# Optimization experiments

Measured on AMD Instinct MI355X. Metric: run time of the kernel, lower is better.

Reference implementation:

```python
import jax, jax.numpy as jnp
import numpy as np

DIM = 384
HEADS = 6
HD = DIM // HEADS
PATCH = 2
FR = 0.5
HEXP = int(HEADS * 4.0)       # attn_proj expanded heads
PR = DIM // 4                  # SQA proj1 out dim
HID = DIM * 4                  # MLP hidden
EPS = 1e-5
SCALE = 1.0 / np.sqrt(HD).astype(np.float32)


def _ln(x, w, b):
    m = jnp.mean(x, axis=-1, keepdims=True)
    v = jnp.var(x, axis=-1, keepdims=True)
    return (x - m) / jnp.sqrt(v + EPS) * w + b


def _lin(x, w, b):
    return x @ w.T + b


def setup_inputs() -> dict:
    key = jax.random.key(0)
    ks = jax.random.split(key, 16)
    def p(i, shape, s=0.02):
        return jax.random.normal(ks[i], shape, jnp.float32) * s
    return {
        "x": jax.random.normal(ks[0], (3136, DIM), jnp.float32),
        "qa": jax.random.normal(ks[1], (1, DIM), jnp.float32),
        "conv_w": p(2, (DIM, 1, 3, 3), 0.1),
        "conv_b": jnp.zeros((DIM,), jnp.float32),
        "norm1_w": jnp.ones((DIM,), jnp.float32),
        "norm1_b": jnp.zeros((DIM,), jnp.float32),
        "norm2_w": jnp.ones((DIM,), jnp.float32),
        "norm2_b": jnp.zeros((DIM,), jnp.float32),
        "qkv_w": p(3, (3 * DIM, DIM)),
        "qkv_b": jnp.zeros((3 * DIM,), jnp.float32),
        "mproj_w": p(4, (DIM, DIM)),
        "mproj_b": jnp.zeros((DIM,), jnp.float32),
        "ap1_w": p(5, (HEXP, HEADS), 0.1),
        "ap1_b": jnp.zeros((HEXP,), jnp.float32),
        "ap2_w": p(6, (HEADS, HEXP), 0.1),
        "ap2_b": jnp.zeros((HEADS,), jnp.float32),
        "kv_w": p(7, (2 * DIM, DIM)),
        "kv_b": jnp.zeros((2 * DIM,), jnp.float32),
        "sp1_w": p(8, (PR, DIM)),
        "sp1_b": jnp.zeros((PR,), jnp.float32),
        "sp2_w": p(9, (DIM, PR)),
        "sp2_b": jnp.zeros((DIM,), jnp.float32),
        "pn_w": jnp.ones((PR,), jnp.float32),
        "pn_b": jnp.zeros((PR,), jnp.float32),
        "fc1_w": p(10, (HID, DIM)),
        "fc1_b": jnp.zeros((HID,), jnp.float32),
        "fc2_w": p(11, (DIM, HID)),
        "fc2_b": jnp.zeros((DIM,), jnp.float32),
    }


def _mmsa(x, qkv_w, qkv_b, mproj_w, mproj_b, ap1_w, ap1_b, ap2_w, ap2_b):
    # x: [S, DIM]
    s = x.shape[0]
    qkv = _lin(x, qkv_w, qkv_b).reshape(s, 3, HEADS, HD).transpose(1, 2, 0, 3)  # [3,h,s,d]
    q, k, v = qkv[0], qkv[1], qkv[2]
    attn = jnp.einsum('hqd,hkd->hqk', q, k) * SCALE           # [h,q,k]
    a = attn.transpose(1, 2, 0)                                # [q,k,h]
    a = a @ ap1_w.T + ap1_b                                    # [q,k,hexp]
    a = jax.nn.softmax(a, axis=1)                              # softmax over k (axis=1)
    a = a @ ap2_w.T + ap2_b                                    # [q,k,h]
    attn = a.transpose(2, 0, 1)                                # [h,q,k]
    out = jnp.einsum('hqk,hkd->hqd', attn, v)
    out = out.transpose(1, 0, 2).reshape(s, DIM)
    return _lin(out, mproj_w, mproj_b)


def _sqa(x, q, kv_w, kv_b, sp1_w, sp1_b, sp2_w, sp2_b, pn_w, pn_b):
    # x: [S, DIM], q: [1, DIM]
    s = x.shape[0]
    qh = q.reshape(1, HEADS, HD).transpose(1, 0, 2)            # [h,1,d]
    kv = _lin(x, kv_w, kv_b).reshape(s, 2, HEADS, HD).transpose(1, 2, 0, 3)
    k, v = kv[0], kv[1]
    attn = jax.nn.softmax(jnp.einsum('hqd,hkd->hqk', qh, k) * SCALE, axis=-1)
    x1 = jnp.einsum('hqk,hkd->hqd', attn, v).transpose(1, 0, 2).reshape(1, DIM)
    x1 = jax.nn.relu(_ln(_lin(x1, sp1_w, sp1_b), pn_w, pn_b))
    x1 = _lin(x1, sp2_w, sp2_b)
    return x + x1                                              # broadcast residual over S


def reference(x, qa, conv_w, conv_b, norm1_w, norm1_b, norm2_w, norm2_b,
              qkv_w, qkv_b, mproj_w, mproj_b, ap1_w, ap1_b, ap2_w, ap2_b,
              kv_w, kv_b, sp1_w, sp1_b, sp2_w, sp2_b, pn_w, pn_b,
              fc1_w, fc1_b, fc2_w, fc2_b):
    L = x.shape[0]
    Hs = int(np.sqrt(L)); Ws = Hs
    # PosCNN2D: depthwise 3x3 conv + residual
    xi = x.T.reshape(1, DIM, Hs, Ws)
    conv = jax.lax.conv_general_dilated(xi, conv_w, (1, 1), 'SAME', feature_group_count=DIM)
    xi = conv + conv_b[None, :, None, None] + xi
    c = xi[0]                                                  # [DIM,Hs,Ws]
    hp, wp = Hs // PATCH, Ws // PATCH
    # 'c (h h1) (w w1) -> (h w) (h1 w1) c'
    x1 = c.reshape(DIM, hp, PATCH, wp, PATCH).transpose(1, 3, 2, 4, 0).reshape(hp * wp, PATCH * PATCH, DIM)
    n = hp * wp
    nf = int(n * FR)
    means = x1.mean(axis=(1, 2))
    idx = jnp.argsort(-means)                                  # descending
    nf_idx, nb_idx = idx[:nf], idx[nf:]
    f = x1[nf_idx].reshape(nf * PATCH * PATCH, DIM)
    b = x1[nb_idx].reshape((n - nf) * PATCH * PATCH, DIM)
    qf = _mmsa(jnp.concatenate([qa, f], axis=0),
               qkv_w, qkv_b, mproj_w, mproj_b, ap1_w, ap1_b, ap2_w, ap2_b)
    qa2, f = qf[:1], qf[1:]
    b = _sqa(b, qa2, kv_w, kv_b, sp1_w, sp1_b, sp2_w, sp2_b, pn_w, pn_b)
    # scatter foreground/background back to patch order
    x1n = jnp.zeros_like(x1)
    x1n = x1n.at[nf_idx].set(f.reshape(nf, PATCH * PATCH, DIM))
    x1n = x1n.at[nb_idx].set(b.reshape(n - nf, PATCH * PATCH, DIM))
    # inverse rearrange '(h w) (h1 w1) c -> ((h h1)(w w1)) c'
    x1f = x1n.reshape(hp, wp, PATCH, PATCH, DIM).transpose(0, 2, 1, 3, 4).reshape(L, DIM)
    x = x + _ln(x1f, norm1_w, norm1_b)
    h = _ln(x, norm2_w, norm2_b)
    h = jax.nn.silu(_lin(h, fc1_w, fc1_b))
    x = x + _lin(h, fc2_w, fc2_b)
    return x, qa2
```

## Files before the change

### kernel.cpp

```cpp
#include <hip/hip_runtime.h>
#include <hip/hip_bf16.h>

#define DIM 384
#define HEADS 6
#define HD 64
#define LPIX 3136
#define HS 56
#define NPATCH 784
#define NF 392
#define SEQ 1569
#define BROWS 1568
#define HEXP 24
#define PR 96
#define HID 1536
#define SCALE 0.125f
#define EPSV 1e-5f
#define KPAD 1576
#define QSTR 9456

typedef short short8v __attribute__((ext_vector_type(8)));
typedef float f32x4 __attribute__((ext_vector_type(4)));
typedef unsigned short ushort;

__device__ __forceinline__ ushort f2b(float f) {
    __hip_bfloat16 h = __float2bfloat16(f);
    return reinterpret_cast<ushort&>(h);
}
__device__ __forceinline__ float b2f(ushort u) {
    unsigned int ui = ((unsigned int)u) << 16;
    return __uint_as_float(ui);
}

struct CvtSeg { const float* s; ushort* d; int n; };
__global__ __launch_bounds__(256) void cvt_kernel(CvtSeg a, CvtSeg b, CvtSeg c, CvtSeg d, CvtSeg e) {
    CvtSeg seg;
    switch (blockIdx.y) { case 0: seg = a; break; case 1: seg = b; break; case 2: seg = c; break;
                          case 3: seg = d; break; default: seg = e; break; }
    int idx = (blockIdx.x * 256 + threadIdx.x) * 8;
    if (idx >= seg.n) return;
    float4 f0 = *reinterpret_cast<const float4*>(seg.s + idx);
    float4 f1 = *reinterpret_cast<const float4*>(seg.s + idx + 4);
    ushort u[8] = { f2b(f0.x), f2b(f0.y), f2b(f0.z), f2b(f0.w),
                    f2b(f1.x), f2b(f1.y), f2b(f1.z), f2b(f1.w) };
    *reinterpret_cast<uint4*>(seg.d + idx) = *reinterpret_cast<uint4*>(u);
}

__global__ __launch_bounds__(384) void conv_kernel(const float* __restrict__ x,
                                                   const float* __restrict__ cw,
                                                   const float* __restrict__ cb,
                                                   float* __restrict__ x1) {
    int l = blockIdx.x, c = threadIdx.x;
    int hh = l / HS, ww = l % HS;
    float acc = x[(long)l * DIM + c] + cb[c];
    #pragma unroll
    for (int kh = 0; kh < 3; kh++) {
        int h2 = hh + kh - 1;
        if (h2 < 0 || h2 >= HS) continue;
        #pragma unroll
        for (int kw = 0; kw < 3; kw++) {
            int w2 = ww + kw - 1;
            if (w2 < 0 || w2 >= HS) continue;
            acc += x[((long)h2 * HS + w2) * DIM + c] * cw[c * 9 + kh * 3 + kw];
        }
    }
    int p = (hh >> 1) * 28 + (ww >> 1);
    int t = ((hh & 1) << 1) | (ww & 1);
    x1[(long)(p * 4 + t) * DIM + c] = acc;
}

__global__ __launch_bounds__(256) void means_kernel(const float* __restrict__ x1, float* __restrict__ means) {
    int p = blockIdx.x, tid = threadIdx.x;
    __shared__ float red[256];
    float s = 0.f;
    for (int i = tid; i < 1536; i += 256) s += x1[(long)p * 1536 + i];
    red[tid] = s; __syncthreads();
    for (int k = 128; k > 0; k >>= 1) { if (tid < k) red[tid] += red[tid + k]; __syncthreads(); }
    if (tid == 0) means[p] = red[0] / 1536.f;
}

__global__ __launch_bounds__(256) void partition_flags_kernel(const float* __restrict__ means, int* __restrict__ flags) {
    int p = blockIdx.x * 256 + threadIdx.x;
    if (p >= NPATCH) return;
    float m = means[p];
    int rank = 0;
    for (int q = 0; q < NPATCH; q++) {
        float mq = means[q];
        rank += (mq > m) || (mq == m && q < p);
    }
    flags[p] = (rank < NF) ? 1 : 0;
}

__global__ __launch_bounds__(256) void partition_compact_kernel(const int* __restrict__ flags, int* __restrict__ isfg,
                                                                int* __restrict__ pos, int* __restrict__ fgmap,
                                                                int* __restrict__ bgmap) {
    __shared__ int f_s[NPATCH];
    __shared__ int scan_s[256];
    int tid = threadIdx.x;
    for (int p = tid; p < NPATCH; p += 256) f_s[p] = flags[p];
    __syncthreads();
    int base = tid * 4, cnt = 0;
    #pragma unroll
    for (int i = 0; i < 4; i++) { int p = base + i; if (p < NPATCH) cnt += f_s[p]; }
    scan_s[tid] = cnt; __syncthreads();
    for (int off = 1; off < 256; off <<= 1) {
        int add = (tid >= off) ? scan_s[tid - off] : 0;
        __syncthreads();
        scan_s[tid] += add;
        __syncthreads();
    }
    int run = scan_s[tid] - cnt;
    for (int i = 0; i < 4; i++) {
        int p = base + i;
        if (p >= NPATCH) break;
        int f = f_s[p];
        if (f) { isfg[p] = 1; pos[p] = run; fgmap[run] = p; run++; }
        else   { isfg[p] = 0; pos[p] = p - run; bgmap[p - run] = p; }
    }
}

__global__ __launch_bounds__(384) void gather_kernel(const float* __restrict__ x1, const float* __restrict__ qa,
                                                     const int* __restrict__ fgmap, const int* __restrict__ bgmap,
                                                     ushort* __restrict__ Xmsa_bf, float* __restrict__ B,
                                                     ushort* __restrict__ B_bf) {
    int c = threadIdx.x;
    int bid = blockIdx.x;
    if (bid == 0) { Xmsa_bf[c] = f2b(qa[c]); return; }
    if (bid <= BROWS) {
        int r = bid - 1;
        int src = fgmap[r >> 2] * 4 + (r & 3);
        Xmsa_bf[(long)bid * DIM + c] = f2b(x1[(long)src * DIM + c]);
    } else {
        int r = bid - SEQ;
        int src = bgmap[r >> 2] * 4 + (r & 3);
        float v = x1[(long)src * DIM + c];
        B[(long)r * DIM + c] = v;
        B_bf[(long)r * DIM + c] = f2b(v);
    }
}

template<int BM, int BN, int OPB, int ACT, int OUTBF>
__global__ __launch_bounds__(256) void mgemm(
    const ushort* __restrict__ A, int lda, long long sA,
    const ushort* __restrict__ B, int ldb, long long sB,
    const float* __restrict__ bias, const float* __restrict__ resid, int ldr,
    void* __restrict__ Cv, int ldc, long long sC,
    int M, int N, int K, float alpha) {
    constexpr int BK = 32, LDT = BK + 8;
    constexpr int WR = (BM == 128 && BN == 128) ? 2 : ((BM == 128) ? 4 : 2);
    constexpr int WC = 4 / WR;
    constexpr int MFR = BM / WR / 16;
    constexpr int NFR = BN / WC / 16;
    __shared__ ushort As[BM * LDT];
    __shared__ ushort Bs[BN * LDT];
    int tid = threadIdx.x;
    int wid = tid >> 6, lane = tid & 63;
    int m0 = blockIdx.y * BM, n0 = blockIdx.x * BN;
    int bz = blockIdx.z;
    A += (long long)bz * sA;
    B += (long long)bz * sB;
    int wm = (wid / WC) * (BM / WR);
    int wn = (wid % WC) * (BN / WC);
    f32x4 acc[MFR][NFR];
    #pragma unroll
    for (int mi = 0; mi < MFR; mi++)
        #pragma unroll
        for (int ni = 0; ni < NFR; ni++) acc[mi][ni] = (f32x4){0.f, 0.f, 0.f, 0.f};

    for (int k0 = 0; k0 < K; k0 += BK) {
        {
            constexpr int CHA = BM * 4 / 256;
            #pragma unroll
            for (int t = 0; t < CHA; t++) {
                int chunk = tid + t * 256;
                int row = chunk >> 2, part = chunk & 3;
                int gm = m0 + row, gk = k0 + part * 8;
                ushort* dst = &As[row * LDT + part * 8];
                if (gm < M && gk + 8 <= K) {
                    *reinterpret_cast<uint4*>(dst) =
                        *reinterpret_cast<const uint4*>(&A[(long long)gm * lda + gk]);
                } else {
                    #pragma unroll
                    for (int i = 0; i < 8; i++) {
                        int k = gk + i;
                        dst[i] = (gm < M && k < K) ? A[(long long)gm * lda + k] : (ushort)0;
                    }
                }
            }
        }
        if (OPB == 1) {
            constexpr int CHB = BN * 4 / 256;
            #pragma unroll
            for (int t = 0; t < CHB; t++) {
                int chunk = tid + t * 256;
                int row = chunk >> 2, part = chunk & 3;
                int gn = n0 + row, gk = k0 + part * 8;
                ushort* dst = &Bs[row * LDT + part * 8];
                if (gn < N && gk + 8 <= K) {
                    *reinterpret_cast<uint4*>(dst) =
                        *reinterpret_cast<const uint4*>(&B[(long long)gn * ldb + gk]);
                } else {
                    #pragma unroll
                    for (int i = 0; i < 8; i++) {
                        int k = gk + i;
                        dst[i] = (gn < N && k < K) ? B[(long long)gn * ldb + k] : (ushort)0;
                    }
                }
            }
        } else {
            int kr = tid >> 3, nn = (tid & 7) * 8;
            int gk = k0 + kr;
            ushort vals[8];
            if (gk < K && n0 + nn + 8 <= N) {
                *reinterpret_cast<uint4*>(vals) =
                    *reinterpret_cast<const uint4*>(&B[(long long)gk * ldb + n0 + nn]);
            } else {
                #pragma unroll
                for (int i = 0; i < 8; i++) {
                    int gn = n0 + nn + i;
                    vals[i] = (gk < K && gn < N) ? B[(long long)gk * ldb + gn] : (ushort)0;
                }
            }
            #pragma unroll
            for (int i = 0; i < 8; i++) Bs[(nn + i) * LDT + kr] = vals[i];
        }
        __syncthreads();
        short8v a[MFR], b[NFR];
        #pragma unroll
        for (int mi = 0; mi < MFR; mi++)
            a[mi] = *reinterpret_cast<const short8v*>(&As[(wm + mi * 16 + (lane & 15)) * LDT + (lane >> 4) * 8]);
        #pragma unroll
        for (int ni = 0; ni < NFR; ni++)
            b[ni] = *reinterpret_cast<const short8v*>(&Bs[(wn + ni * 16 + (lane & 15)) * LDT + (lane >> 4) * 8]);
        #pragma unroll
        for (int mi = 0; mi < MFR; mi++)
            #pragma unroll
            for (int ni = 0; ni < NFR; ni++)
                acc[mi][ni] = __builtin_amdgcn_mfma_f32_16x16x32_bf16(a[mi], b[ni], acc[mi][ni], 0, 0, 0);
        __syncthreads();
    }
    ushort* C16 = (ushort*)Cv;
    float* C32 = (float*)Cv;
    #pragma unroll
    for (int mi = 0; mi < MFR; mi++) {
        #pragma unroll
        for (int j = 0; j < 4; j++) {
            int gm = m0 + wm + mi * 16 + (lane >> 4) * 4 + j;
            if (gm >= M) continue;
            #pragma unroll
            for (int ni = 0; ni < NFR; ni++) {
                int gn = n0 + wn + ni * 16 + (lane & 15);
                if (gn >= N) continue;
                float v = acc[mi][ni][j] * alpha;
                if (bias) v += bias[gn];
                if (ACT == 1) v = v / (1.f + __expf(-v));
                if (resid) v += resid[(long long)gm * ldr + gn];
                long long ci = bz * sC + (long long)gm * ldc + gn;
                if (OUTBF) C16[ci] = f2b(v); else C32[ci] = v;
            }
        }
    }
}

__global__ __launch_bounds__(512, 2) void modattn_kernel(
    ushort* __restrict__ S,
    const float* __restrict__ ap1_w, const float* __restrict__ ap1_b,
    const float* __restrict__ ap2_w, const float* __restrict__ ap2_b) {
    int q = blockIdx.x, tid = threadIdx.x;
    int wid = tid >> 6, lane = tid & 63;
    __shared__ float w1s[144], w2s[144], b1s[24], b2s[6];
    __shared__ float red[8][24];
    __shared__ float fin[24];
    if (tid < 144) { w1s[tid] = ap1_w[tid]; w2s[tid] = ap2_w[tid]; }
    if (tid < 24) b1s[tid] = ap1_b[tid];
    if (tid < 6)  b2s[tid] = ap2_b[tid];
    __syncthreads();
    ushort* Sq = S + (long long)q * QSTR;
    float sreg[4][6];
    #pragma unroll
    for (int j = 0; j < 4; j++) {
        int k = tid + j * 512;
        #pragma unroll
        for (int h = 0; h < 6; h++)
            sreg[j][h] = (k < SEQ) ? b2f(Sq[h * KPAD + k]) : 0.f;
    }
    float a1[4][24];
    float r24[24];
    #pragma unroll
    for (int e = 0; e < 24; e++) r24[e] = -3.4e38f;
    #pragma unroll
    for (int j = 0; j < 4; j++) {
        int k = tid + j * 512;
        bool v = k < SEQ;
        #pragma unroll
        for (int e = 0; e < 24; e++) {
            float a = b1s[e];
            #pragma unroll
            for (int h = 0; h < 6; h++) a = fmaf(sreg[j][h], w1s[e * 6 + h], a);
            a1[j][e] = a;
            if (v) r24[e] = fmaxf(r24[e], a);
        }
    }
    #pragma unroll
    for (int e = 0; e < 24; e++) {
        float v = r24[e];
        #pragma unroll
        for (int off = 32; off >= 1; off >>= 1) v = fmaxf(v, __shfl_xor(v, off));
        r24[e] = v;
    }
    if (lane == 0) {
        #pragma unroll
        for (int e = 0; e < 24; e++) red[wid][e] = r24[e];
    }
    __syncthreads();
    if (tid < 24) {
        float v = red[0][tid];
        #pragma unroll
        for (int w = 1; w < 8; w++) v = fmaxf(v, red[w][tid]);
        fin[tid] = v;
    }
    __syncthreads();
    #pragma unroll
    for (int e = 0; e < 24; e++) r24[e] = 0.f;
    #pragma unroll
    for (int j = 0; j < 4; j++) {
        int k = tid + j * 512;
        bool v = k < SEQ;
        #pragma unroll
        for (int e = 0; e < 24; e++) {
            float p = v ? __expf(a1[j][e] - fin[e]) : 0.f;
            a1[j][e] = p;
            r24[e] += p;
        }
    }
    #pragma unroll
    for (int e = 0; e < 24; e++) {
        float v = r24[e];
        #pragma unroll
        for (int off = 32; off >= 1; off >>= 1) v += __shfl_xor(v, off);
        r24[e] = v;
    }
    __syncthreads();
    if (lane == 0) {
        #pragma unroll
        for (int e = 0; e < 24; e++) red[wid][e] = r24[e];
    }
    __syncthreads();
    if (tid < 24) {
        float v = red[0][tid];
        #pragma unroll
        for (int w = 1; w < 8; w++) v += red[w][tid];
        fin[tid] = 1.f / v;
    }
    __syncthreads();
    #pragma unroll
    for (int j = 0; j < 4; j++) {
        int k = tid + j * 512;
        if (k >= SEQ) continue;
        float a2[6];
        #pragma unroll
        for (int h = 0; h < 6; h++) a2[h] = b2s[h];
        #pragma unroll
        for (int e = 0; e < 24; e++) {
            float p = a1[j][e] * fin[e];
            #pragma unroll
            for (int h = 0; h < 6; h++) a2[h] = fmaf(p, w2s[h * 24 + e], a2[h]);
        }
        #pragma unroll
        for (int h = 0; h < 6; h++) Sq[h * KPAD + k] = f2b(a2[h]);
    }
}

__global__ __launch_bounds__(256) void sqa_attn_kernel(const float* __restrict__ kv, const float* __restrict__ qa2,
                                                       float* __restrict__ x1h) {
    int h = blockIdx.x, tid = threadIdx.x;
    __shared__ float q_s[HD];
    __shared__ float l_s[BROWS];
    __shared__ float red[256];
    if (tid < HD) q_s[tid] = qa2[h * HD + tid];
    __syncthreads();
    float lmax = -1e30f;
    for (int s = tid; s < BROWS; s += 256) {
        const float* krow = kv + (long long)s * 768 + h * HD;
        float d = 0.f;
        for (int i = 0; i < HD; i++) d += krow[i] * q_s[i];
        d *= SCALE; l_s[s] = d; lmax = fmaxf(lmax, d);
    }
    red[tid] = lmax; __syncthreads();
    for (int s = 128; s > 0; s >>= 1) { if (tid < s) red[tid] = fmaxf(red[tid], red[tid + s]); __syncthreads(); }
    float gmax = red[0]; __syncthreads();
    float lsum = 0.f;
    for (int s = tid; s < BROWS; s += 256) { float p = __expf(l_s[s] - gmax); l_s[s] = p; lsum += p; }
    red[tid] = lsum; __syncthreads();
    for (int s = 128; s > 0; s >>= 1) { if (tid < s) red[tid] += red[tid + s]; __syncthreads(); }
    float inv = 1.f / red[0]; __syncthreads();
    int d = tid & 63, g = tid >> 6;
    float acc = 0.f;
    for (int s = g; s < BROWS; s += 4) acc += l_s[s] * kv[(long long)s * 768 + 384 + h * HD + d];
    red[tid] = acc; __syncthreads();
    if (tid < HD) x1h[h * HD + d] = (red[d] + red[64 + d] + red[128 + d] + red[192 + d]) * inv;
}

__global__ __launch_bounds__(384) void sqa_mlp_kernel(const float* __restrict__ x1h,
                                                      const float* __restrict__ sp1_w, const float* __restrict__ sp1_b,
                                                      const float* __restrict__ pn_w, const float* __restrict__ pn_b,
                                                      const float* __restrict__ sp2_w, const float* __restrict__ sp2_b,
                                                      float* __restrict__ z) {
    __shared__ float y_s[PR];
    __shared__ float x_s[DIM];
    __shared__ float mv[2];
    int tid = threadIdx.x;
    x_s[tid] = x1h[tid];
    __syncthreads();
    if (tid < PR) {
        float a = sp1_b[tid];
        for (int c = 0; c < DIM; c++) a += sp1_w[tid * DIM + c] * x_s[c];
        y_s[tid] = a;
    }
    __syncthreads();
    if (tid == 0) {
        float m = 0.f; for (int i = 0; i < PR; i++) m += y_s[i]; m /= (float)PR;
        float v = 0.f; for (int i = 0; i < PR; i++) { float d = y_s[i] - m; v += d * d; } v /= (float)PR;
        mv[0] = m; mv[1] = rsqrtf(v + EPSV);
    }
    __syncthreads();
    if (tid < PR) {
        float yn = (y_s[tid] - mv[0]) * mv[1] * pn_w[tid] + pn_b[tid];
        y_s[tid] = fmaxf(yn, 0.f);
    }
    __syncthreads();
    float a = sp2_b[tid];
    for (int j = 0; j < PR; j++) a += sp2_w[tid * PR + j] * y_s[j];
    z[tid] = a;
}

__global__ __launch_bounds__(384) void scatter_ln_kernel(
    const float* __restrict__ x, const float* __restrict__ mpout, const float* __restrict__ B,
    const float* __restrict__ z, const int* __restrict__ isfg, const int* __restrict__ pos,
    const float* __restrict__ n1w, const float* __restrict__ n1b,
    const float* __restrict__ n2w, const float* __restrict__ n2b,
    float* __restrict__ x_mid, ushort* __restrict__ hnorm_bf) {
    int l = blockIdx.x, c = threadIdx.x;
    int wid = c >> 6, lane = c & 63;
    int hh = l / HS, ww = l % HS;
    int p = (hh >> 1) * 28 + (ww >> 1);
    int t = ((hh & 1) << 1) | (ww & 1);
    float v;
    if (isfg[p]) v = mpout[(long long)(1 + pos[p] * 4 + t) * DIM + c];
    else v = B[(long long)(pos[p] * 4 + t) * DIM + c] + z[c];
    __shared__ float r0[8], r1[8], r2[8], r3[8];
    float s1 = v, s2 = v * v;
    #pragma unroll
    for (int off = 32; off >= 1; off >>= 1) { s1 += __shfl_xor(s1, off); s2 += __shfl_xor(s2, off); }
    if (lane == 0) { r0[wid] = s1; r1[wid] = s2; }
    __syncthreads();
    float mean = (r0[0] + r0[1] + r0[2] + r0[3] + r0[4] + r0[5]) / (float)DIM;
    float var = (r1[0] + r1[1] + r1[2] + r1[3] + r1[4] + r1[5]) / (float)DIM - mean * mean;
    float xm = x[(long long)l * DIM + c] + (v - mean) * rsqrtf(var + EPSV) * n1w[c] + n1b[c];
    x_mid[(long long)l * DIM + c] = xm;
    s1 = xm; s2 = xm * xm;
    #pragma unroll
    for (int off = 32; off >= 1; off >>= 1) { s1 += __shfl_xor(s1, off); s2 += __shfl_xor(s2, off); }
    if (lane == 0) { r2[wid] = s1; r3[wid] = s2; }
    __syncthreads();
    float m2 = (r2[0] + r2[1] + r2[2] + r2[3] + r2[4] + r2[5]) / (float)DIM;
    float v2 = (r3[0] + r3[1] + r3[2] + r3[3] + r3[4] + r3[5]) / (float)DIM - m2 * m2;
    hnorm_bf[(long long)l * DIM + c] = f2b((xm - m2) * rsqrtf(v2 + EPSV) * n2w[c] + n2b[c]);
}

__global__ void copy_qa2_kernel(const float* __restrict__ mp, float* __restrict__ dst) {
    dst[threadIdx.x] = mp[threadIdx.x];
}

extern "C" void kernel_launch(void* const* d_in, const int* in_sizes, int n_in,
                              void* d_out, int out_size, void* d_ws, size_t ws_size,
                              hipStream_t stream) {
    const float* x       = (const float*)d_in[0];
    const float* qa      = (const float*)d_in[1];
    const float* conv_w  = (const float*)d_in[2];
    const float* conv_b  = (const float*)d_in[3];
    const float* n1w     = (const float*)d_in[4];
    const float* n1b     = (const float*)d_in[5];
    const float* n2w     = (const float*)d_in[6];
    const float* n2b     = (const float*)d_in[7];
    const float* qkv_w   = (const float*)d_in[8];
    const float* qkv_b   = (const float*)d_in[9];
    const float* mproj_w = (const float*)d_in[10];
    const float* mproj_b = (const float*)d_in[11];
    const float* ap1_w   = (const float*)d_in[12];
    const float* ap1_b   = (const float*)d_in[13];
    const float* ap2_w   = (const float*)d_in[14];
    const float* ap2_b   = (const float*)d_in[15];
    const float* kv_w    = (const float*)d_in[16];
    const float* kv_b    = (const float*)d_in[17];
    const float* sp1_w   = (const float*)d_in[18];
    const float* sp1_b   = (const float*)d_in[19];
    const float* sp2_w   = (const float*)d_in[20];
    const float* sp2_b   = (const float*)d_in[21];
    const float* pn_w    = (const float*)d_in[22];
    const float* pn_b    = (const float*)d_in[23];
    const float* fc1_w   = (const float*)d_in[24];
    const float* fc1_b   = (const float*)d_in[25];
    const float* fc2_w   = (const float*)d_in[26];
    const float* fc2_b   = (const float*)d_in[27];
    float* out = (float*)d_out;
    float* ws  = (float*)d_ws;

    const long long X1_OFF    = 0;
    const long long BMAT_OFF  = 1204224;
    const long long S_OFF     = 1806336;
    const long long MPOUT_OFF = 16576912;
    const long long XMID_OFF  = 17179408;
    const long long WBF_OFF   = 18383632;
    const long long MEANS_OFF = 19415824;
    const long long X1H_OFF   = 19416608;
    const long long Z_OFF     = 19416992;
    const long long FLAGS_OFF = 19417376;
    const long long ISFG_OFF  = 19418160;
    const long long POS_OFF   = 19418944;
    const long long FGMAP_OFF = 19419728;
    const long long BGMAP_OFF = 19420120;

    float*  x1_arr  = ws + X1_OFF;
    float*  Bmat    = ws + BMAT_OFF;
    float*  mpout   = ws + MPOUT_OFF;
    float*  xmid    = ws + XMID_OFF;
    float*  means   = ws + MEANS_OFF;
    float*  x1h     = ws + X1H_OFF;
    float*  zvec    = ws + Z_OFF;
    int*    flags   = (int*)(ws + FLAGS_OFF);
    int*    isfg    = (int*)(ws + ISFG_OFF);
    int*    pos     = (int*)(ws + POS_OFF);
    int*    fgmap   = (int*)(ws + FGMAP_OFF);
    int*    bgmap   = (int*)(ws + BGMAP_OFF);

    ushort* S16     = (ushort*)(ws + S_OFF);
    ushort* qkvb_bf = (ushort*)(ws + X1_OFF);
    ushort* Xmsa_bf = (ushort*)(ws + MPOUT_OFF);
    ushort* Bmat_bf = (ushort*)(ws + XMID_OFF);
    ushort* attn_bf = (ushort*)(ws + XMID_OFF + 301056);
    float*  kv_out  = ws + S_OFF;
    ushort* hnorm_bf= (ushort*)(ws + S_OFF + 1204224);
    ushort* hact_bf = (ushort*)(ws + S_OFF + 1806336);

    ushort* wbf      = (ushort*)(ws + WBF_OFF);
    ushort* qkvw_bf  = wbf;
    ushort* mprojw_bf= wbf + 442368;
    ushort* kvw_bf   = wbf + 589824;
    ushort* fc1w_bf  = wbf + 884736;
    ushort* fc2w_bf  = wbf + 1474560;

    {
        CvtSeg s0{qkv_w, qkvw_bf, 442368};
        CvtSeg s1{mproj_w, mprojw_bf, 147456};
        CvtSeg s2{kv_w, kvw_bf, 294912};
        CvtSeg s3{fc1_w, fc1w_bf, 589824};
        CvtSeg s4{fc2_w, fc2w_bf, 589824};
        dim3 g(288, 5, 1);
        cvt_kernel<<<g, 256, 0, stream>>>(s0, s1, s2, s3, s4);
    }

    conv_kernel<<<LPIX, 384, 0, stream>>>(x, conv_w, conv_b, x1_arr);
    means_kernel<<<NPATCH, 256, 0, stream>>>(x1_arr, means);
    partition_flags_kernel<<<4, 256, 0, stream>>>(means, flags);
    partition_compact_kernel<<<1, 256, 0, stream>>>(flags, isfg, pos, fgmap, bgmap);
    gather_kernel<<<SEQ + BROWS, 384, 0, stream>>>(x1_arr, qa, fgmap, bgmap, Xmsa_bf, Bmat, Bmat_bf);

    {
        dim3 g(18, 25, 1);
        mgemm<64,64,1,0,1><<<g, 256, 0, stream>>>(Xmsa_bf, DIM, 0, qkvw_bf, DIM, 0, qkv_b,
                                                  nullptr, 0, qkvb_bf, 1152, 0, SEQ, 1152, DIM, 1.f);
    }
    {
        dim3 g(13, 13, 6);
        mgemm<128,128,1,0,1><<<g, 256, 0, stream>>>(qkvb_bf, 1152, 64, qkvb_bf + 384, 1152, 64, nullptr,
                                                    nullptr, 0, S16, QSTR, (long long)KPAD, SEQ, SEQ, HD, SCALE);
    }
    modattn_kernel<<<SEQ, 512, 0, stream>>>(S16, ap1_w, ap1_b, ap2_w, ap2_b);
    {
        dim3 g(1, 25, 6);
        mgemm<64,64,0,0,1><<<g, 256, 0, stream>>>(S16, QSTR, (long long)KPAD, qkvb_bf + 768, 1152, 64, nullptr,
                                                  nullptr, 0, attn_bf, DIM, 64, SEQ, HD, SEQ, 1.f);
    }
    {
        dim3 g(6, 25, 1);
        mgemm<64,64,1,0,0><<<g, 256, 0, stream>>>(attn_bf, DIM, 0, mprojw_bf, DIM, 0, mproj_b,
                                                  nullptr, 0, mpout, DIM, 0, SEQ, DIM, DIM, 1.f);
    }
    {
        dim3 g(12, 25, 1);
        mgemm<64,64,1,0,0><<<g, 256, 0, stream>>>(Bmat_bf, DIM, 0, kvw_bf, DIM, 0, kv_b,
                                                  nullptr, 0, kv_out, 768, 0, BROWS, 768, DIM, 1.f);
    }
    sqa_attn_kernel<<<HEADS, 256, 0, stream>>>(kv_out, mpout , x1h);
    sqa_mlp_kernel<<<1, 384, 0, stream>>>(x1h, sp1_w, sp1_b, pn_w, pn_b, sp2_w, sp2_b, zvec);
    scatter_ln_kernel<<<LPIX, 384, 0, stream>>>(x, mpout, Bmat, zvec, isfg, pos,
                                                n1w, n1b, n2w, n2b, xmid, hnorm_bf);
    {
        dim3 g(12, 25, 1);
        mgemm<128,128,1,1,1><<<g, 256, 0, stream>>>(hnorm_bf, DIM, 0, fc1w_bf, DIM, 0, fc1_b,
                                                    nullptr, 0, hact_bf, HID, 0, LPIX, HID, DIM, 1.f);
    }
    {
        dim3 g(6, 50, 1);
        mgemm<64,64,1,0,0><<<g, 256, 0, stream>>>(hact_bf, HID, 0, fc2w_bf, HID, 0, fc2_b,
                                                  xmid, DIM, out, DIM, 0, LPIX, DIM, HID, 1.f);
    }
    copy_qa2_kernel<<<1, 384, 0, stream>>>(mpout, out + (long long)LPIX * DIM);
}
```

Before: 623.3 us.

## Fuse patch means into conv, merge partition kernels, restructure modattn and SQA attention

Patch means are now accumulated with atomics inside the conv kernel, replacing the separate means kernel. The rank and compaction kernels merge into one 1024-thread block, and the qa2 copy folds into the SQA MLP kernel, cutting kernel launches. The modulated-attention kernel stages its score row in LDS, processes the 24 expanded heads in two halves to lower register pressure, and is declared for higher occupancy. SQA attention moves to 512 threads with float4 loads and wave-shuffle reductions. Atomic float accumulation makes the means, and so the top-k ordering on ties, nondeterministic.

```diff
diff --git a/kernel.cpp b/kernel.cpp
--- a/kernel.cpp
+++ b/kernel.cpp
@@ -48,8 +48,10 @@
 __global__ __launch_bounds__(384) void conv_kernel(const float* __restrict__ x,
                                                    const float* __restrict__ cw,
                                                    const float* __restrict__ cb,
-                                                   float* __restrict__ x1) {
+                                                   float* __restrict__ x1,
+                                                   float* __restrict__ means) {
     int l = blockIdx.x, c = threadIdx.x;
+    int wid = c >> 6, lane = c & 63;
     int hh = l / HS, ww = l % HS;
     float acc = x[(long)l * DIM + c] + cb[c];
     #pragma unroll
@@ -66,55 +68,60 @@
     int p = (hh >> 1) * 28 + (ww >> 1);
     int t = ((hh & 1) << 1) | (ww & 1);
     x1[(long)(p * 4 + t) * DIM + c] = acc;
-}
-
-__global__ __launch_bounds__(256) void means_kernel(const float* __restrict__ x1, float* __restrict__ means) {
-    int p = blockIdx.x, tid = threadIdx.x;
-    __shared__ float red[256];
-    float s = 0.f;
-    for (int i = tid; i < 1536; i += 256) s += x1[(long)p * 1536 + i];
-    red[tid] = s; __syncthreads();
-    for (int k = 128; k > 0; k >>= 1) { if (tid < k) red[tid] += red[tid + k]; __syncthreads(); }
-    if (tid == 0) means[p] = red[0] / 1536.f;
-}
-
-__global__ __launch_bounds__(256) void partition_flags_kernel(const float* __restrict__ means, int* __restrict__ flags) {
-    int p = blockIdx.x * 256 + threadIdx.x;
-    if (p >= NPATCH) return;
-    float m = means[p];
-    int rank = 0;
-    for (int q = 0; q < NPATCH; q++) {
-        float mq = means[q];
-        rank += (mq > m) || (mq == m && q < p);
-    }
-    flags[p] = (rank < NF) ? 1 : 0;
-}
-
-__global__ __launch_bounds__(256) void partition_compact_kernel(const int* __restrict__ flags, int* __restrict__ isfg,
-                                                                int* __restrict__ pos, int* __restrict__ fgmap,
-                                                                int* __restrict__ bgmap) {
-    __shared__ int f_s[NPATCH];
+    float s = acc;
+    #pragma unroll
+    for (int off = 32; off >= 1; off >>= 1) s += __shfl_xor(s, off);
+    __shared__ float wred[6];
+    if (lane == 0) wred[wid] = s;
+    __syncthreads();
+    if (c == 0) atomicAdd(&means[p], wred[0] + wred[1] + wred[2] + wred[3] + wred[4] + wred[5]);
+}
+
+__global__ __launch_bounds__(1024) void partition_kernel(const float* __restrict__ means, int* __restrict__ isfg,
+                                                         int* __restrict__ pos, int* __restrict__ fgmap,
+                                                         int* __restrict__ bgmap) {
+    __shared__ float m_s[NPATCH];
+    __shared__ unsigned char flag_s[NPATCH];
     __shared__ int scan_s[256];
     int tid = threadIdx.x;
-    for (int p = tid; p < NPATCH; p += 256) f_s[p] = flags[p];
-    __syncthreads();
-    int base = tid * 4, cnt = 0;
-    #pragma unroll
-    for (int i = 0; i < 4; i++) { int p = base + i; if (p < NPATCH) cnt += f_s[p]; }
-    scan_s[tid] = cnt; __syncthreads();
+    if (tid < NPATCH) m_s[tid] = means[tid];
+    __syncthreads();
+    if (tid < NPATCH) {
+        float m = m_s[tid];
+        int rank = 0;
+        for (int q2 = 0; q2 < NPATCH; q2++) {
+            float mq = m_s[q2];
+            rank += (mq > m) || (mq == m && q2 < tid);
+        }
+        flag_s[tid] = (rank < NF) ? 1 : 0;
+    }
+    __syncthreads();
+    if (tid < 256) {
+        int base = tid * 4, cnt = 0;
+        #pragma unroll
+        for (int i = 0; i < 4; i++) { int p = base + i; if (p < NPATCH) cnt += flag_s[p]; }
+        scan_s[tid] = cnt;
+    }
+    __syncthreads();
     for (int off = 1; off < 256; off <<= 1) {
-        int add = (tid >= off) ? scan_s[tid - off] : 0;
-        __syncthreads();
-        scan_s[tid] += add;
-        __syncthreads();
-    }
-    int run = scan_s[tid] - cnt;
-    for (int i = 0; i < 4; i++) {
-        int p = base + i;
-        if (p >= NPATCH) break;
-        int f = f_s[p];
-        if (f) { isfg[p] = 1; pos[p] = run; fgmap[run] = p; run++; }
-        else   { isfg[p] = 0; pos[p] = p - run; bgmap[p - run] = p; }
+        int add = 0;
+        if (tid < 256 && tid >= off) add = scan_s[tid - off];
+        __syncthreads();
+        if (tid < 256) scan_s[tid] += add;
+        __syncthreads();
+    }
+    if (tid < 256) {
+        int base = tid * 4, cnt = 0;
+        #pragma unroll
+        for (int i = 0; i < 4; i++) { int p = base + i; if (p < NPATCH) cnt += flag_s[p]; }
+        int run = scan_s[tid] - cnt;
+        for (int i = 0; i < 4; i++) {
+            int p = base + i;
+            if (p >= NPATCH) break;
+            int f = flag_s[p];
+            if (f) { isfg[p] = 1; pos[p] = run; fgmap[run] = p; run++; }
+            else   { isfg[p] = 0; pos[p] = p - run; bgmap[p - run] = p; }
+        }
     }
 }
 
@@ -261,154 +268,228 @@
     }
 }
 
-__global__ __launch_bounds__(512, 2) void modattn_kernel(
+__global__ __launch_bounds__(512, 4) void modattn_kernel(
     ushort* __restrict__ S,
     const float* __restrict__ ap1_w, const float* __restrict__ ap1_b,
     const float* __restrict__ ap2_w, const float* __restrict__ ap2_b) {
     int q = blockIdx.x, tid = threadIdx.x;
     int wid = tid >> 6, lane = tid & 63;
+    __shared__ ushort s_lds[6 * KPAD];
     __shared__ float w1s[144], w2s[144], b1s[24], b2s[6];
-    __shared__ float red[8][24];
-    __shared__ float fin[24];
+    __shared__ float red[8][12];
+    __shared__ float fin[12];
     if (tid < 144) { w1s[tid] = ap1_w[tid]; w2s[tid] = ap2_w[tid]; }
     if (tid < 24) b1s[tid] = ap1_b[tid];
     if (tid < 6)  b2s[tid] = ap2_b[tid];
-    __syncthreads();
-    ushort* Sq = S + (long long)q * QSTR;
-    float sreg[4][6];
+    {
+        const uint4* g = reinterpret_cast<const uint4*>(S + (long long)q * QSTR);
+        uint4* l = reinterpret_cast<uint4*>(s_lds);
+        #pragma unroll
+        for (int t = 0; t < 3; t++) {
+            int i = tid + t * 512;
+            if (i < 1182) l[i] = g[i];
+        }
+    }
+    __syncthreads();
+    float a2acc[4][6];
+    #pragma unroll
+    for (int j = 0; j < 4; j++)
+        #pragma unroll
+        for (int h = 0; h < 6; h++) a2acc[j][h] = b2s[h];
+
+    #pragma unroll
+    for (int c = 0; c < 2; c++) {
+        float a1[4][12];
+        float r12[12];
+        #pragma unroll
+        for (int e = 0; e < 12; e++) r12[e] = -3.4e38f;
+        #pragma unroll
+        for (int j = 0; j < 4; j++) {
+            int k = tid + j * 512;
+            bool val = k < SEQ;
+            int kc = val ? k : 0;
+            float sv[6];
+            #pragma unroll
+            for (int h = 0; h < 6; h++) sv[h] = b2f(s_lds[h * KPAD + kc]);
+            #pragma unroll
+            for (int e = 0; e < 12; e++) {
+                int eg = c * 12 + e;
+                float a = b1s[eg];
+                #pragma unroll
+                for (int h = 0; h < 6; h++) a = fmaf(sv[h], w1s[eg * 6 + h], a);
+                a1[j][e] = a;
+                if (val) r12[e] = fmaxf(r12[e], a);
+            }
+        }
+        #pragma unroll
+        for (int e = 0; e < 12; e++) {
+            float v = r12[e];
+            #pragma unroll
+            for (int off = 32; off >= 1; off >>= 1) v = fmaxf(v, __shfl_xor(v, off));
+            r12[e] = v;
+        }
+        if (lane == 0) {
+            #pragma unroll
+            for (int e = 0; e < 12; e++) red[wid][e] = r12[e];
+        }
+        __syncthreads();
+        if (tid < 12) {
+            float v = red[0][tid];
+            #pragma unroll
+            for (int w = 1; w < 8; w++) v = fmaxf(v, red[w][tid]);
+            fin[tid] = v;
+        }
+        __syncthreads();
+        #pragma unroll
+        for (int e = 0; e < 12; e++) r12[e] = 0.f;
+        #pragma unroll
+        for (int j = 0; j < 4; j++) {
+            int k = tid + j * 512;
+            bool val = k < SEQ;
+            #pragma unroll
+            for (int e = 0; e < 12; e++) {
+                float p = val ? __expf(a1[j][e] - fin[e]) : 0.f;
+                a1[j][e] = p;
+                r12[e] += p;
+            }
+        }
+        #pragma unroll
+        for (int e = 0; e < 12; e++) {
+            float v = r12[e];
+            #pragma unroll
+            for (int off = 32; off >= 1; off >>= 1) v += __shfl_xor(v, off);
+            r12[e] = v;
+        }
+        if (lane == 0) {
+            #pragma unroll
+            for (int e = 0; e < 12; e++) red[wid][e] = r12[e];
+        }
+        __syncthreads();
+        if (tid < 12) {
+            float v = red[0][tid];
+            #pragma unroll
+            for (int w = 1; w < 8; w++) v += red[w][tid];
+            fin[tid] = 1.f / v;
+        }
+        __syncthreads();
+        #pragma unroll
+        for (int j = 0; j < 4; j++) {
+            #pragma unroll
+            for (int e = 0; e < 12; e++) {
+                float p = a1[j][e] * fin[e];
+                int eg = c * 12 + e;
+                #pragma unroll
+                for (int h = 0; h < 6; h++) a2acc[j][h] = fmaf(p, w2s[h * 24 + eg], a2acc[j][h]);
+            }
+        }
+    }
     #pragma unroll
     for (int j = 0; j < 4; j++) {
         int k = tid + j * 512;
-        #pragma unroll
-        for (int h = 0; h < 6; h++)
-            sreg[j][h] = (k < SEQ) ? b2f(Sq[h * KPAD + k]) : 0.f;
-    }
-    float a1[4][24];
-    float r24[24];
-    #pragma unroll
-    for (int e = 0; e < 24; e++) r24[e] = -3.4e38f;
-    #pragma unroll
-    for (int j = 0; j < 4; j++) {
-        int k = tid + j * 512;
-        bool v = k < SEQ;
-        #pragma unroll
-        for (int e = 0; e < 24; e++) {
-            float a = b1s[e];
-            #pragma unroll
-            for (int h = 0; h < 6; h++) a = fmaf(sreg[j][h], w1s[e * 6 + h], a);
-            a1[j][e] = a;
-            if (v) r24[e] = fmaxf(r24[e], a);
-        }
-    }
-    #pragma unroll
-    for (int e = 0; e < 24; e++) {
-        float v = r24[e];
-        #pragma unroll
-        for (int off = 32; off >= 1; off >>= 1) v = fmaxf(v, __shfl_xor(v, off));
-        r24[e] = v;
-    }
-    if (lane == 0) {
-        #pragma unroll
-        for (int e = 0; e < 24; e++) red[wid][e] = r24[e];
-    }
-    __syncthreads();
-    if (tid < 24) {
-        float v = red[0][tid];
-        #pragma unroll
-        for (int w = 1; w < 8; w++) v = fmaxf(v, red[w][tid]);
-        fin[tid] = v;
-    }
-    __syncthreads();
-    #pragma unroll
-    for (int e = 0; e < 24; e++) r24[e] = 0.f;
-    #pragma unroll
-    for (int j = 0; j < 4; j++) {
-        int k = tid + j * 512;
-        bool v = k < SEQ;
-        #pragma unroll
-        for (int e = 0; e < 24; e++) {
-            float p = v ? __expf(a1[j][e] - fin[e]) : 0.f;
-            a1[j][e] = p;
-            r24[e] += p;
-        }
-    }
-    #pragma unroll
-    for (int e = 0; e < 24; e++) {
-        float v = r24[e];
-        #pragma unroll
-        for (int off = 32; off >= 1; off >>= 1) v += __shfl_xor(v, off);
-        r24[e] = v;
-    }
-    __syncthreads();
-    if (lane == 0) {
-        #pragma unroll
-        for (int e = 0; e < 24; e++) red[wid][e] = r24[e];
-    }
-    __syncthreads();
-    if (tid < 24) {
-        float v = red[0][tid];
-        #pragma unroll
-        for (int w = 1; w < 8; w++) v += red[w][tid];
-        fin[tid] = 1.f / v;
-    }
-    __syncthreads();
-    #pragma unroll
-    for (int j = 0; j < 4; j++) {
-        int k = tid + j * 512;
-        if (k >= SEQ) continue;
-        float a2[6];
-        #pragma unroll
-        for (int h = 0; h < 6; h++) a2[h] = b2s[h];
-        #pragma unroll
-        for (int e = 0; e < 24; e++) {
-            float p = a1[j][e] * fin[e];
-            #pragma unroll
-            for (int h = 0; h < 6; h++) a2[h] = fmaf(p, w2s[h * 24 + e], a2[h]);
-        }
-        #pragma unroll
-        for (int h = 0; h < 6; h++) Sq[h * KPAD + k] = f2b(a2[h]);
-    }
-}
-
-__global__ __launch_bounds__(256) void sqa_attn_kernel(const float* __restrict__ kv, const float* __restrict__ qa2,
+        if (k < SEQ) {
+            #pragma unroll
+            for (int h = 0; h < 6; h++) s_lds[h * KPAD + k] = f2b(a2acc[j][h]);
+        } else if (k < KPAD) {
+            #pragma unroll
+            for (int h = 0; h < 6; h++) s_lds[h * KPAD + k] = 0;
+        }
+    }
+    __syncthreads();
+    {
+        const uint4* l = reinterpret_cast<const uint4*>(s_lds);
+        uint4* g = reinterpret_cast<uint4*>(S + (long long)q * QSTR);
+        #pragma unroll
+        for (int t = 0; t < 3; t++) {
+            int i = tid + t * 512;
+            if (i < 1182) g[i] = l[i];
+        }
+    }
+}
+
+__global__ __launch_bounds__(512) void sqa_attn_kernel(const float* __restrict__ kv, const float* __restrict__ qa2,
                                                        float* __restrict__ x1h) {
     int h = blockIdx.x, tid = threadIdx.x;
+    int wid = tid >> 6, lane = tid & 63;
     __shared__ float q_s[HD];
     __shared__ float l_s[BROWS];
-    __shared__ float red[256];
+    __shared__ float red8[8];
+    __shared__ float pvred[8][HD];
+    __shared__ float gmv;
     if (tid < HD) q_s[tid] = qa2[h * HD + tid];
     __syncthreads();
     float lmax = -1e30f;
-    for (int s = tid; s < BROWS; s += 256) {
-        const float* krow = kv + (long long)s * 768 + h * HD;
-        float d = 0.f;
-        for (int i = 0; i < HD; i++) d += krow[i] * q_s[i];
-        d *= SCALE; l_s[s] = d; lmax = fmaxf(lmax, d);
-    }
-    red[tid] = lmax; __syncthreads();
-    for (int s = 128; s > 0; s >>= 1) { if (tid < s) red[tid] = fmaxf(red[tid], red[tid + s]); __syncthreads(); }
-    float gmax = red[0]; __syncthreads();
+    #pragma unroll
+    for (int j = 0; j < 4; j++) {
+        int s = tid + j * 512;
+        if (s < BROWS) {
+            const float4* kr = reinterpret_cast<const float4*>(kv + (long long)s * 768 + h * HD);
+            float d = 0.f;
+            #pragma unroll
+            for (int i = 0; i < 16; i++) {
+                float4 f = kr[i];
+                d = fmaf(f.x, q_s[i * 4 + 0], d); d = fmaf(f.y, q_s[i * 4 + 1], d);
+                d = fmaf(f.z, q_s[i * 4 + 2], d); d = fmaf(f.w, q_s[i * 4 + 3], d);
+            }
+            d *= SCALE;
+            l_s[s] = d;
+            lmax = fmaxf(lmax, d);
+        }
+    }
+    #pragma unroll
+    for (int off = 32; off >= 1; off >>= 1) lmax = fmaxf(lmax, __shfl_xor(lmax, off));
+    if (lane == 0) red8[wid] = lmax;
+    __syncthreads();
+    if (tid == 0) {
+        float v = red8[0];
+        #pragma unroll
+        for (int w = 1; w < 8; w++) v = fmaxf(v, red8[w]);
+        gmv = v;
+    }
+    __syncthreads();
+    float gmax = gmv;
     float lsum = 0.f;
-    for (int s = tid; s < BROWS; s += 256) { float p = __expf(l_s[s] - gmax); l_s[s] = p; lsum += p; }
-    red[tid] = lsum; __syncthreads();
-    for (int s = 128; s > 0; s >>= 1) { if (tid < s) red[tid] += red[tid + s]; __syncthreads(); }
-    float inv = 1.f / red[0]; __syncthreads();
+    #pragma unroll
+    for (int j = 0; j < 4; j++) {
+        int s = tid + j * 512;
+        if (s < BROWS) { float p = __expf(l_s[s] - gmax); l_s[s] = p; lsum += p; }
+    }
+    #pragma unroll
+    for (int off = 32; off >= 1; off >>= 1) lsum += __shfl_xor(lsum, off);
+    if (lane == 0) red8[wid] = lsum;
+    __syncthreads();
+    if (tid == 0) {
+        float v = 0.f;
+        #pragma unroll
+        for (int w = 0; w < 8; w++) v += red8[w];
+        gmv = 1.f / v;
+    }
+    __syncthreads();
+    float inv = gmv;
     int d = tid & 63, g = tid >> 6;
     float acc = 0.f;
-    for (int s = g; s < BROWS; s += 4) acc += l_s[s] * kv[(long long)s * 768 + 384 + h * HD + d];
-    red[tid] = acc; __syncthreads();
-    if (tid < HD) x1h[h * HD + d] = (red[d] + red[64 + d] + red[128 + d] + red[192 + d]) * inv;
+    for (int s = g; s < BROWS; s += 8)
+        acc = fmaf(l_s[s], kv[(long long)s * 768 + 384 + h * HD + d], acc);
+    pvred[g][d] = acc;
+    __syncthreads();
+    if (tid < HD) {
+        float v = 0.f;
+        #pragma unroll
+        for (int w = 0; w < 8; w++) v += pvred[w][tid];
+        x1h[h * HD + tid] = v * inv;
+    }
 }
 
 __global__ __launch_bounds__(384) void sqa_mlp_kernel(const float* __restrict__ x1h,
                                                       const float* __restrict__ sp1_w, const float* __restrict__ sp1_b,
                                                       const float* __restrict__ pn_w, const float* __restrict__ pn_b,
                                                       const float* __restrict__ sp2_w, const float* __restrict__ sp2_b,
-                                                      float* __restrict__ z) {
+                                                      float* __restrict__ z,
+                                                      const float* __restrict__ mp, float* __restrict__ dq) {
     __shared__ float y_s[PR];
     __shared__ float x_s[DIM];
     __shared__ float mv[2];
     int tid = threadIdx.x;
+    dq[tid] = mp[tid];
     x_s[tid] = x1h[tid];
     __syncthreads();
     if (tid < PR) {
@@ -465,10 +546,6 @@
     float m2 = (r2[0] + r2[1] + r2[2] + r2[3] + r2[4] + r2[5]) / (float)DIM;
     float v2 = (r3[0] + r3[1] + r3[2] + r3[3] + r3[4] + r3[5]) / (float)DIM - m2 * m2;
     hnorm_bf[(long long)l * DIM + c] = f2b((xm - m2) * rsqrtf(v2 + EPSV) * n2w[c] + n2b[c]);
-}
-
-__global__ void copy_qa2_kernel(const float* __restrict__ mp, float* __restrict__ dst) {
-    dst[threadIdx.x] = mp[threadIdx.x];
 }
 
 extern "C" void kernel_launch(void* const* d_in, const int* in_sizes, int n_in,
@@ -514,7 +591,6 @@
     const long long MEANS_OFF = 19415824;
     const long long X1H_OFF   = 19416608;
     const long long Z_OFF     = 19416992;
-    const long long FLAGS_OFF = 19417376;
     const long long ISFG_OFF  = 19418160;
     const long long POS_OFF   = 19418944;
     const long long FGMAP_OFF = 19419728;
@@ -527,7 +603,6 @@
     float*  means   = ws + MEANS_OFF;
     float*  x1h     = ws + X1H_OFF;
     float*  zvec    = ws + Z_OFF;
-    int*    flags   = (int*)(ws + FLAGS_OFF);
     int*    isfg    = (int*)(ws + ISFG_OFF);
     int*    pos     = (int*)(ws + POS_OFF);
     int*    fgmap   = (int*)(ws + FGMAP_OFF);
@@ -559,10 +634,9 @@
         cvt_kernel<<<g, 256, 0, stream>>>(s0, s1, s2, s3, s4);
     }
 
-    conv_kernel<<<LPIX, 384, 0, stream>>>(x, conv_w, conv_b, x1_arr);
-    means_kernel<<<NPATCH, 256, 0, stream>>>(x1_arr, means);
-    partition_flags_kernel<<<4, 256, 0, stream>>>(means, flags);
-    partition_compact_kernel<<<1, 256, 0, stream>>>(flags, isfg, pos, fgmap, bgmap);
+    hipMemsetAsync(means, 0, NPATCH * sizeof(float), stream);
+    conv_kernel<<<LPIX, 384, 0, stream>>>(x, conv_w, conv_b, x1_arr, means);
+    partition_kernel<<<1, 1024, 0, stream>>>(means, isfg, pos, fgmap, bgmap);
     gather_kernel<<<SEQ + BROWS, 384, 0, stream>>>(x1_arr, qa, fgmap, bgmap, Xmsa_bf, Bmat, Bmat_bf);
 
     {
@@ -591,8 +665,9 @@
         mgemm<64,64,1,0,0><<<g, 256, 0, stream>>>(Bmat_bf, DIM, 0, kvw_bf, DIM, 0, kv_b,
                                                   nullptr, 0, kv_out, 768, 0, BROWS, 768, DIM, 1.f);
     }
-    sqa_attn_kernel<<<HEADS, 256, 0, stream>>>(kv_out, mpout , x1h);
-    sqa_mlp_kernel<<<1, 384, 0, stream>>>(x1h, sp1_w, sp1_b, pn_w, pn_b, sp2_w, sp2_b, zvec);
+    sqa_attn_kernel<<<HEADS, 512, 0, stream>>>(kv_out, mpout , x1h);
+    sqa_mlp_kernel<<<1, 384, 0, stream>>>(x1h, sp1_w, sp1_b, pn_w, pn_b, sp2_w, sp2_b, zvec,
+                                          mpout, out + (long long)LPIX * DIM);
     scatter_ln_kernel<<<LPIX, 384, 0, stream>>>(x, mpout, Bmat, zvec, isfg, pos,
                                                 n1w, n1b, n2w, n2b, xmid, hnorm_bf);
     {
@@ -605,5 +680,4 @@
         mgemm<64,64,1,0,0><<<g, 256, 0, stream>>>(hact_bf, HID, 0, fc2w_bf, HID, 0, fc2_b,
                                                   xmid, DIM, out, DIM, 0, LPIX, DIM, HID, 1.f);
     }
-    copy_qa2_kernel<<<1, 384, 0, stream>>>(mpout, out + (long long)LPIX * DIM);
-}
+}
```

After: 699.1 us. +12.2%, slower.
